# Optimization experiments

Hardware: AMD Instinct MI355X
Metric: run time of the kernel (lower is better)

Reference implementation:

```python
import jax, jax.numpy as jnp
import numpy as np

B, T, I, O = 64, 1024, 512, 512
EPS = 1e-5


def setup_inputs() -> dict:
    key = jax.random.key(0)
    k1, k2 = jax.random.split(key)
    x = jax.random.normal(k1, (B, T, I), dtype=jnp.float32)
    W = jax.random.normal(k2, (4 * O, I + O), dtype=jnp.float32) * 0.02
    gamma = jnp.ones((4, O), dtype=jnp.float32)
    beta = jnp.zeros((4, O), dtype=jnp.float32)
    init_hx = jnp.zeros((1, O), dtype=jnp.float32)
    init_cx = jnp.zeros((1, O), dtype=jnp.float32)
    return {"x": x, "W": W, "gamma": gamma, "beta": beta,
            "init_hx": init_hx, "init_cx": init_cx}


def reference(x, W, gamma, beta, init_hx, init_cx):
    b = x.shape[0]
    o = init_hx.shape[-1]

    def step(carry, xt):
        h, c = carry
        # fused gate projection: [B, I+O] @ [I+O, 4O] -> [B, 4, O]
        z = jnp.concatenate([xt, h], axis=-1) @ W.T
        z = z.reshape(b, 4, o)
        # LayerNorm over the last TWO dims (gate axis + feature axis), per torch nn.LayerNorm([4, O])
        mu = jnp.mean(z, axis=(-2, -1), keepdims=True)
        var = jnp.var(z, axis=(-2, -1), keepdims=True)
        zn = (z - mu) * jax.lax.rsqrt(var + EPS) * gamma + beta
        gates = jax.nn.sigmoid(zn[:, :3])  # f, i, o gates
        f_g, i_g, o_g = gates[:, 0], gates[:, 1], gates[:, 2]
        h_state = jax.nn.gelu(zn[:, 3], approximate=False)  # dropout = identity (eval)
        c_new = f_g * c + i_g * h_state
        h_new = o_g * c_new
        return (h_new, c_new), h_new

    h0 = jnp.broadcast_to(init_hx, (b, o))
    c0 = jnp.broadcast_to(init_cx, (b, o))
    x_t = jnp.swapaxes(x, 0, 1)  # [T, B, I]
    _, hs = jax.lax.scan(step, (h0, c0), x_t)
    return jnp.swapaxes(hs, 0, 1)  # [B, T, O]
```

## Files before the change

### kernel.cpp

```cpp
#include <hip/hip_runtime.h>
#include <math.h>

#define B_  64
#define T_  1024
#define I_  512
#define O_  512
#define NZ  2048
#define KW  1024
#define EPS 1e-5f

#define SREC 32
#define OSL  16

typedef short bf8_t  __attribute__((ext_vector_type(8)));
typedef float f32x4  __attribute__((ext_vector_type(4)));
typedef unsigned uint4v __attribute__((ext_vector_type(4)));

__device__ __forceinline__ unsigned short f2bf(float f) {
  union { float f; unsigned u; } v; v.f = f;
  unsigned r = v.u + 0x7FFFu + ((v.u >> 16) & 1u);
  return (unsigned short)(r >> 16);
}
__device__ __forceinline__ float bf2f(unsigned short b) {
  union { unsigned u; float f; } v; v.u = ((unsigned)b) << 16;
  return v.f;
}

__global__ __launch_bounds__(256) void init_all(
    const float* __restrict__ init_hx,
    unsigned short* __restrict__ h, unsigned* __restrict__ sync) {
  int idx = blockIdx.x * 256 + threadIdx.x;
  if (idx < 2048) sync[idx] = 0u;
  if (idx < B_ * O_) h[idx] = f2bf(init_hx[idx & (O_ - 1)]);
}

__global__ __launch_bounds__(256) void wx_bf16(
    const float* __restrict__ W, unsigned short* __restrict__ Wbf) {
  int idx = blockIdx.x * 256 + threadIdx.x;
  int n  = idx >> 7;
  int k4 = (idx & 127) * 4;
  float4 v = *(const float4*)(W + (size_t)n * KW + k4);
  unsigned short* d = Wbf + (size_t)n * 512 + k4;
  d[0] = f2bf(v.x); d[1] = f2bf(v.y); d[2] = f2bf(v.z); d[3] = f2bf(v.w);
}

__global__ __launch_bounds__(256) void zx_gemm(
    const float* __restrict__ x, const unsigned short* __restrict__ Wbf,
    unsigned short* __restrict__ zx) {
  __shared__ unsigned short xl[64 * 520];
  __shared__ unsigned short cst[64 * 72];

  const int tid  = threadIdx.x;
  const int w    = tid >> 6;
  const int lane = tid & 63;
  const int q    = lane >> 4;
  const int col  = lane & 15;
  const int m0   = blockIdx.x * 64;

  for (int e4 = tid; e4 < 64 * 128; e4 += 256) {
    int r  = e4 >> 7;
    int k4 = (e4 & 127) * 4;
    float4 v = *(const float4*)(x + (size_t)(m0 + r) * I_ + k4);
    unsigned short* d = &xl[r * 520 + k4];
    d[0] = f2bf(v.x); d[1] = f2bf(v.y); d[2] = f2bf(v.z); d[3] = f2bf(v.w);
  }
  __syncthreads();

  const unsigned short* __restrict__ arow = &xl[(16 * w + col) * 520];
  const int crow = tid >> 2;
  const int cc0  = (tid & 3) * 16;

  for (int nblk = 0; nblk < 32; ++nblk) {
    const int n0 = nblk * 64;
    f32x4 acc[4];
    #pragma unroll
    for (int i = 0; i < 4; ++i) acc[i] = (f32x4){0.f, 0.f, 0.f, 0.f};

    #pragma unroll
    for (int ks = 0; ks < 16; ++ks) {
      const int k0 = ks * 32 + q * 8;
      bf8_t af = *(const bf8_t*)(arow + k0);
      #pragma unroll
      for (int nt = 0; nt < 4; ++nt) {
        bf8_t bfr = *(const bf8_t*)(Wbf + (size_t)(n0 + nt * 16 + col) * 512 + k0);
        acc[nt] = __builtin_amdgcn_mfma_f32_16x16x32_bf16(af, bfr, acc[nt], 0, 0, 0);
      }
    }
    __syncthreads();
    #pragma unroll
    for (int nt = 0; nt < 4; ++nt)
      #pragma unroll
      for (int r = 0; r < 4; ++r)
        cst[(16 * w + 4 * q + r) * 72 + nt * 16 + col] = f2bf(acc[nt][r]);
    __syncthreads();
    {
      const uint4v* srcp = (const uint4v*)&cst[crow * 72 + cc0];
      uint4v v0 = srcp[0], v1 = srcp[1];
      uint4v* dst = (uint4v*)&zx[(size_t)(m0 + crow) * NZ + n0 + cc0];
      dst[0] = v0; dst[1] = v1;
    }
  }
}

__global__ __launch_bounds__(256) void lstm_rec(
    const float* __restrict__ W, const float* __restrict__ gamma,
    const float* __restrict__ beta, const float* __restrict__ init_cx,
    const unsigned short* __restrict__ zx, unsigned short* __restrict__ h,
    unsigned long long* __restrict__ part8, float* __restrict__ out,
    unsigned* __restrict__ flags) {

  __shared__ unsigned short whlds[64 * 520];

  const int tid  = threadIdx.x;
  const int w    = tid >> 6;
  const int lane = tid & 63;
  const int q    = lane >> 4;
  const int col  = lane & 15;
  const int s    = blockIdx.x;
  const int o    = s * OSL + col;

  for (int e4 = tid; e4 < 64 * 128; e4 += 256) {
    int r  = e4 >> 7;
    int k4 = (e4 & 127) * 4;
    int g  = r >> 4, np = r & 15;
    const float4 v =
        *(const float4*)(W + (size_t)(512 * g + OSL * s + np) * KW + I_ + k4);
    unsigned short* d = &whlds[r * 520 + k4];
    d[0] = f2bf(v.x); d[1] = f2bf(v.y); d[2] = f2bf(v.z); d[3] = f2bf(v.w);
  }

  float gma[4], bta[4], c_reg[4];
  #pragma unroll
  for (int g = 0; g < 4; ++g) { gma[g] = gamma[g * O_ + o]; bta[g] = beta[g * O_ + o]; }
  { float c0 = init_cx[o];
    #pragma unroll
    for (int r = 0; r < 4; ++r) c_reg[r] = c0; }

  unsigned short zxl[16];
  #pragma unroll
  for (int g = 0; g < 4; ++g)
    #pragma unroll
    for (int r = 0; r < 4; ++r) {
      int b = 16 * w + 4 * q + r;
      zxl[g * 4 + r] = zx[((size_t)b * T_ + 0) * NZ + g * O_ + OSL * s + col];
    }

  __syncthreads();

  for (int t = 0; t < T_; ++t) {
    unsigned long long araw[32];
    const unsigned short* hrow = h + (16 * w + col) * O_;
    #pragma unroll
    for (int ks = 0; ks < 16; ++ks) {
      const unsigned long long* p =
          (const unsigned long long*)(hrow + ks * 32 + q * 8);
      araw[2 * ks]     = __hip_atomic_load(p,     __ATOMIC_RELAXED, __HIP_MEMORY_SCOPE_AGENT);
      araw[2 * ks + 1] = __hip_atomic_load(p + 1, __ATOMIC_RELAXED, __HIP_MEMORY_SCOPE_AGENT);
    }

    f32x4 acc[4];
    #pragma unroll
    for (int g = 0; g < 4; ++g) acc[g] = (f32x4){0.f, 0.f, 0.f, 0.f};

    #pragma unroll
    for (int ks = 0; ks < 16; ++ks) {
      union { unsigned long long u[2]; bf8_t v; } au;
      au.u[0] = araw[2 * ks]; au.u[1] = araw[2 * ks + 1];
      #pragma unroll
      for (int g = 0; g < 4; ++g) {
        bf8_t bfr = *(const bf8_t*)(&whlds[(g * 16 + col) * 520 + ks * 32 + q * 8]);
        acc[g] = __builtin_amdgcn_mfma_f32_16x16x32_bf16(au.v, bfr, acc[g], 0, 0, 0);
      }
    }

    float z[16];
    float s1[4], s2[4];
    #pragma unroll
    for (int r = 0; r < 4; ++r) { s1[r] = 0.f; s2[r] = 0.f; }
    #pragma unroll
    for (int g = 0; g < 4; ++g)
      #pragma unroll
      for (int r = 0; r < 4; ++r) {
        float zv = acc[g][r] + bf2f(zxl[g * 4 + r]);
        z[g * 4 + r] = zv;
        s1[r] += zv;
        s2[r] += zv * zv;
      }
    #pragma unroll
    for (int m = 1; m < 16; m <<= 1) {
      #pragma unroll
      for (int r = 0; r < 4; ++r) {
        s1[r] += __shfl_xor(s1[r], m, 64);
        s2[r] += __shfl_xor(s2[r], m, 64);
      }
    }
    if (col == 0) {
      #pragma unroll
      for (int r = 0; r < 4; ++r) {
        int b = 16 * w + 4 * q + r;
        union { float f[2]; unsigned long long u; } pv;
        pv.f[0] = s1[r]; pv.f[1] = s2[r];
        __hip_atomic_store(&part8[(size_t)s * 64 + b], pv.u,
                           __ATOMIC_RELAXED, __HIP_MEMORY_SCOPE_AGENT);
      }
    }

    __syncthreads();
    {
      const unsigned tgt = 2u * (unsigned)t + 1u;
      if (tid == 0)
        __hip_atomic_store(&flags[s * 16], tgt,
                           __ATOMIC_RELAXED, __HIP_MEMORY_SCOPE_AGENT);
      const unsigned* fp = &flags[(tid & 31) * 16];
      while (__hip_atomic_load(fp, __ATOMIC_RELAXED, __HIP_MEMORY_SCOPE_AGENT) < tgt) {}
    }

    float S1 = 0.f, S2 = 0.f;
    {
      const int brow = 16 * w + (lane & 15);
      const int sbase = (lane >> 4) * 8;
      #pragma unroll
      for (int i = 0; i < 8; ++i) {
        union { float f[2]; unsigned long long u; } pv;
        pv.u = __hip_atomic_load(&part8[(size_t)(sbase + i) * 64 + brow],
                                 __ATOMIC_RELAXED, __HIP_MEMORY_SCOPE_AGENT);
        S1 += pv.f[0]; S2 += pv.f[1];
      }
    }
    S1 += __shfl_xor(S1, 16, 64); S2 += __shfl_xor(S2, 16, 64);
    S1 += __shfl_xor(S1, 32, 64); S2 += __shfl_xor(S2, 32, 64);
    float mean_l = S1 * (1.f / NZ);
    float rstd_l = rsqrtf(S2 * (1.f / NZ) - mean_l * mean_l + EPS);

    float hnl[4];
    #pragma unroll
    for (int r = 0; r < 4; ++r) {
      int b = 16 * w + 4 * q + r;
      float mean = __shfl(mean_l, 4 * q + r, 64);
      float rstd = __shfl(rstd_l, 4 * q + r, 64);
      float zn0 = (z[0 * 4 + r] - mean) * rstd * gma[0] + bta[0];
      float zn1 = (z[1 * 4 + r] - mean) * rstd * gma[1] + bta[1];
      float zn2 = (z[2 * 4 + r] - mean) * rstd * gma[2] + bta[2];
      float zn3 = (z[3 * 4 + r] - mean) * rstd * gma[3] + bta[3];
      float fg = 1.f / (1.f + expf(-zn0));
      float ig = 1.f / (1.f + expf(-zn1));
      float og = 1.f / (1.f + expf(-zn2));
      float gg = 0.5f * zn3 * (1.f + erff(zn3 * 0.70710678118654752f));
      float cn = fg * c_reg[r] + ig * gg;
      float hn = og * cn;
      c_reg[r] = cn;
      hnl[r] = hn;
      __hip_atomic_store(&h[b * O_ + o], f2bf(hn),
                         __ATOMIC_RELAXED, __HIP_MEMORY_SCOPE_AGENT);
    }

    if (t + 1 < T_) {
      __syncthreads();
      const unsigned tgt = 2u * (unsigned)t + 2u;
      if (tid == 0)
        __hip_atomic_store(&flags[s * 16], tgt,
                           __ATOMIC_RELAXED, __HIP_MEMORY_SCOPE_AGENT);
      #pragma unroll
      for (int r = 0; r < 4; ++r) {
        int b = 16 * w + 4 * q + r;
        out[((size_t)b * T_ + t) * O_ + o] = hnl[r];
      }
      #pragma unroll
      for (int g = 0; g < 4; ++g)
        #pragma unroll
        for (int r = 0; r < 4; ++r) {
          int b = 16 * w + 4 * q + r;
          zxl[g * 4 + r] =
              zx[((size_t)b * T_ + (t + 1)) * NZ + g * O_ + OSL * s + col];
        }
      const unsigned* fp = &flags[(tid & 31) * 16];
      while (__hip_atomic_load(fp, __ATOMIC_RELAXED, __HIP_MEMORY_SCOPE_AGENT) < tgt) {}
    } else {
      #pragma unroll
      for (int r = 0; r < 4; ++r) {
        int b = 16 * w + 4 * q + r;
        out[((size_t)b * T_ + t) * O_ + o] = hnl[r];
      }
    }
  }
}

extern "C" void kernel_launch(void* const* d_in, const int* in_sizes, int n_in,
                              void* d_out, int out_size, void* d_ws, size_t ws_size,
                              hipStream_t stream) {
  const float* x       = (const float*)d_in[0];
  const float* W       = (const float*)d_in[1];
  const float* gamma   = (const float*)d_in[2];
  const float* beta    = (const float*)d_in[3];
  const float* init_hx = (const float*)d_in[4];
  const float* init_cx = (const float*)d_in[5];
  float* out = (float*)d_out;
  (void)in_sizes; (void)n_in; (void)out_size; (void)ws_size;

  char* ws = (char*)d_ws;
  unsigned*           flags = (unsigned*)(ws);
  unsigned long long* part8 = (unsigned long long*)(ws + 8192);
  unsigned short*     h     = (unsigned short*)(ws + 32768);
  unsigned short*     Wbf   = (unsigned short*)(ws + (1 << 20));
  unsigned short*     zx    = (unsigned short*)(ws + (4 << 20));

  init_all<<<128, 256, 0, stream>>>(init_hx, h, flags);
  wx_bf16<<<1024, 256, 0, stream>>>(W, Wbf);
  zx_gemm<<<1024, 256, 0, stream>>>(x, Wbf, zx);
  lstm_rec<<<SREC, 256, 0, stream>>>(W, gamma, beta, init_cx, zx, h, part8, out, flags);
}
```

Baseline: 9.497 ms.

## Replace flag barrier for LayerNorm stats with self-validating tagged packets

```diff
diff --git a/kernel.cpp b/kernel.cpp
--- a/kernel.cpp
+++ b/kernel.cpp
@@ -11,6 +11,7 @@
 
 #define SREC 32
 #define OSL  16
+#define BAILOUT (1u << 18)
 
 typedef short bf8_t  __attribute__((ext_vector_type(8)));
 typedef float f32x4  __attribute__((ext_vector_type(4)));
@@ -25,12 +26,17 @@
   union { unsigned u; float f; } v; v.u = ((unsigned)b) << 16;
   return v.f;
 }
+__device__ __forceinline__ float u2f(unsigned u) {
+  union { unsigned u; float f; } v; v.u = u; return v.f;
+}
 
 __global__ __launch_bounds__(256) void init_all(
     const float* __restrict__ init_hx,
-    unsigned short* __restrict__ h, unsigned* __restrict__ sync) {
+    unsigned short* __restrict__ h, unsigned* __restrict__ sync,
+    unsigned* __restrict__ part16) {
   int idx = blockIdx.x * 256 + threadIdx.x;
   if (idx < 2048) sync[idx] = 0u;
+  if (idx < 8192) part16[idx] = 0u;
   if (idx < B_ * O_) h[idx] = f2bf(init_hx[idx & (O_ - 1)]);
 }
 
@@ -106,7 +112,7 @@
     const float* __restrict__ W, const float* __restrict__ gamma,
     const float* __restrict__ beta, const float* __restrict__ init_cx,
     const unsigned short* __restrict__ zx, unsigned short* __restrict__ h,
-    unsigned long long* __restrict__ part8, float* __restrict__ out,
+    unsigned* __restrict__ part16, float* __restrict__ out,
     unsigned* __restrict__ flags) {
 
   __shared__ unsigned short whlds[64 * 520];
@@ -194,38 +200,55 @@
         s2[r] += __shfl_xor(s2[r], m, 64);
       }
     }
+
+    const unsigned tgt = (unsigned)t + 1u;
+
     if (col == 0) {
       #pragma unroll
       for (int r = 0; r < 4; ++r) {
         int b = 16 * w + 4 * q + r;
-        union { float f[2]; unsigned long long u; } pv;
-        pv.f[0] = s1[r]; pv.f[1] = s2[r];
-        __hip_atomic_store(&part8[(size_t)s * 64 + b], pv.u,
-                           __ATOMIC_RELAXED, __HIP_MEMORY_SCOPE_AGENT);
-      }
-    }
-
-    __syncthreads();
-    {
-      const unsigned tgt = 2u * (unsigned)t + 1u;
-      if (tid == 0)
-        __hip_atomic_store(&flags[s * 16], tgt,
-                           __ATOMIC_RELAXED, __HIP_MEMORY_SCOPE_AGENT);
-      const unsigned* fp = &flags[(tid & 31) * 16];
-      while (__hip_atomic_load(fp, __ATOMIC_RELAXED, __HIP_MEMORY_SCOPE_AGENT) < tgt) {}
+        uint4v pkt;
+        pkt[0] = tgt;
+        pkt[1] = __builtin_bit_cast(unsigned, s1[r]);
+        pkt[2] = __builtin_bit_cast(unsigned, s2[r]);
+        pkt[3] = tgt;
+        unsigned* pp = part16 + (size_t)(s * 64 + b) * 4;
+        asm volatile("global_store_dwordx4 %0, %1, off sc1"
+                     :: "v"(pp), "v"(pkt) : "memory");
+      }
     }
 
     float S1 = 0.f, S2 = 0.f;
     {
-      const int brow = 16 * w + (lane & 15);
-      const int sbase = (lane >> 4) * 8;
-      #pragma unroll
-      for (int i = 0; i < 8; ++i) {
-        union { float f[2]; unsigned long long u; } pv;
-        pv.u = __hip_atomic_load(&part8[(size_t)(sbase + i) * 64 + brow],
-                                 __ATOMIC_RELAXED, __HIP_MEMORY_SCOPE_AGENT);
-        S1 += pv.f[0]; S2 += pv.f[1];
-      }
+      const int brow = 16 * w + col;
+      const unsigned* pb  = part16 + ((size_t)q * 512 + brow) * 4;
+      const unsigned* pb2 = pb + 1024;
+      uint4v pk[8];
+      unsigned spins = 0;
+      bool ok;
+      do {
+        asm volatile(
+          "global_load_dwordx4 %0, %8, off sc1\n\t"
+          "global_load_dwordx4 %1, %8, off offset:1024 sc1\n\t"
+          "global_load_dwordx4 %2, %8, off offset:2048 sc1\n\t"
+          "global_load_dwordx4 %3, %8, off offset:3072 sc1\n\t"
+          "global_load_dwordx4 %4, %9, off sc1\n\t"
+          "global_load_dwordx4 %5, %9, off offset:1024 sc1\n\t"
+          "global_load_dwordx4 %6, %9, off offset:2048 sc1\n\t"
+          "global_load_dwordx4 %7, %9, off offset:3072 sc1\n\t"
+          "s_waitcnt vmcnt(0)"
+          : "=&v"(pk[0]), "=&v"(pk[1]), "=&v"(pk[2]), "=&v"(pk[3]),
+            "=&v"(pk[4]), "=&v"(pk[5]), "=&v"(pk[6]), "=&v"(pk[7])
+          : "v"(pb), "v"(pb2)
+          : "memory");
+        ok = true;
+        #pragma unroll
+        for (int i = 0; i < 8; ++i)
+          ok = ok && (pk[i][0] == tgt) && (pk[i][3] == tgt);
+        if (++spins > BAILOUT) break;
+      } while (!__all((int)ok));
+      #pragma unroll
+      for (int i = 0; i < 8; ++i) { S1 += u2f(pk[i][1]); S2 += u2f(pk[i][2]); }
     }
     S1 += __shfl_xor(S1, 16, 64); S2 += __shfl_xor(S2, 16, 64);
     S1 += __shfl_xor(S1, 32, 64); S2 += __shfl_xor(S2, 32, 64);
@@ -256,9 +279,9 @@
 
     if (t + 1 < T_) {
       __syncthreads();
-      const unsigned tgt = 2u * (unsigned)t + 2u;
+      const unsigned ft = 2u * (unsigned)t + 2u;
       if (tid == 0)
-        __hip_atomic_store(&flags[s * 16], tgt,
+        __hip_atomic_store(&flags[s * 16], ft,
                            __ATOMIC_RELAXED, __HIP_MEMORY_SCOPE_AGENT);
       #pragma unroll
       for (int r = 0; r < 4; ++r) {
@@ -274,7 +297,7 @@
               zx[((size_t)b * T_ + (t + 1)) * NZ + g * O_ + OSL * s + col];
         }
       const unsigned* fp = &flags[(tid & 31) * 16];
-      while (__hip_atomic_load(fp, __ATOMIC_RELAXED, __HIP_MEMORY_SCOPE_AGENT) < tgt) {}
+      while (__hip_atomic_load(fp, __ATOMIC_RELAXED, __HIP_MEMORY_SCOPE_AGENT) < ft) {}
     } else {
       #pragma unroll
       for (int r = 0; r < 4; ++r) {
@@ -298,14 +321,14 @@
   (void)in_sizes; (void)n_in; (void)out_size; (void)ws_size;
 
   char* ws = (char*)d_ws;
-  unsigned*           flags = (unsigned*)(ws);
-  unsigned long long* part8 = (unsigned long long*)(ws + 8192);
-  unsigned short*     h     = (unsigned short*)(ws + 32768);
-  unsigned short*     Wbf   = (unsigned short*)(ws + (1 << 20));
-  unsigned short*     zx    = (unsigned short*)(ws + (4 << 20));
-
-  init_all<<<128, 256, 0, stream>>>(init_hx, h, flags);
+  unsigned*       flags  = (unsigned*)(ws);
+  unsigned*       part16 = (unsigned*)(ws + 8192);
+  unsigned short* h      = (unsigned short*)(ws + 49152);
+  unsigned short* Wbf    = (unsigned short*)(ws + (1 << 20));
+  unsigned short* zx     = (unsigned short*)(ws + (4 << 20));
+
+  init_all<<<128, 256, 0, stream>>>(init_hx, h, flags, part16);
   wx_bf16<<<1024, 256, 0, stream>>>(W, Wbf);
   zx_gemm<<<1024, 256, 0, stream>>>(x, Wbf, zx);
-  lstm_rec<<<SREC, 256, 0, stream>>>(W, gamma, beta, init_cx, zx, h, part8, out, flags);
-}
+  lstm_rec<<<SREC, 256, 0, stream>>>(W, gamma, beta, init_cx, zx, h, part16, out, flags);
+}
```

Result: slower. 9.802 ms (+3.2%).

## Fuse input-projection GEMM with recurrence kernel and overlap via per-chunk counters

Applied to the files above, without the earlier changes.

```diff
diff --git a/kernel.cpp b/kernel.cpp
--- a/kernel.cpp
+++ b/kernel.cpp
@@ -10,7 +10,9 @@
 #define EPS 1e-5f
 
 #define SREC 32
+#define NPROD 1024
 #define OSL  16
+#define BAILOUT (1u << 18)
 
 typedef short bf8_t  __attribute__((ext_vector_type(8)));
 typedef float f32x4  __attribute__((ext_vector_type(4)));
@@ -44,80 +46,90 @@
   d[0] = f2bf(v.x); d[1] = f2bf(v.y); d[2] = f2bf(v.z); d[3] = f2bf(v.w);
 }
 
-__global__ __launch_bounds__(256) void zx_gemm(
+__global__ __launch_bounds__(256) void fused_rec(
     const float* __restrict__ x, const unsigned short* __restrict__ Wbf,
-    unsigned short* __restrict__ zx) {
-  __shared__ unsigned short xl[64 * 520];
-  __shared__ unsigned short cst[64 * 72];
+    const float* __restrict__ W, const float* __restrict__ gamma,
+    const float* __restrict__ beta, const float* __restrict__ init_cx,
+    unsigned short* __restrict__ zx, unsigned short* __restrict__ h,
+    unsigned long long* __restrict__ part8, float* __restrict__ out,
+    unsigned* __restrict__ flags) {
+
+  __shared__ unsigned short smem[37888];
 
   const int tid  = threadIdx.x;
   const int w    = tid >> 6;
   const int lane = tid & 63;
   const int q    = lane >> 4;
   const int col  = lane & 15;
-  const int m0   = blockIdx.x * 64;
-
-  for (int e4 = tid; e4 < 64 * 128; e4 += 256) {
-    int r  = e4 >> 7;
-    int k4 = (e4 & 127) * 4;
-    float4 v = *(const float4*)(x + (size_t)(m0 + r) * I_ + k4);
-    unsigned short* d = &xl[r * 520 + k4];
-    d[0] = f2bf(v.x); d[1] = f2bf(v.y); d[2] = f2bf(v.z); d[3] = f2bf(v.w);
+  unsigned* zxcnt = flags + 1024;
+
+  if (blockIdx.x >= SREC) {
+    const int p  = blockIdx.x - SREC;
+    const int b  = p & 63;
+    const int tc = p >> 6;
+    const int m0 = b * T_ + tc * 64;
+
+    unsigned short* xl  = smem;
+    unsigned short* cst = smem + 33280;
+
+    for (int e4 = tid; e4 < 64 * 128; e4 += 256) {
+      int r  = e4 >> 7;
+      int k4 = (e4 & 127) * 4;
+      float4 v = *(const float4*)(x + (size_t)(m0 + r) * I_ + k4);
+      unsigned short* d = &xl[r * 520 + k4];
+      d[0] = f2bf(v.x); d[1] = f2bf(v.y); d[2] = f2bf(v.z); d[3] = f2bf(v.w);
+    }
+    __syncthreads();
+
+    const unsigned short* arow = &xl[(16 * w + col) * 520];
+    const int crow = tid >> 2;
+    const int cc0  = (tid & 3) * 16;
+
+    for (int nblk = 0; nblk < 32; ++nblk) {
+      const int n0 = nblk * 64;
+      f32x4 acc[4];
+      #pragma unroll
+      for (int i = 0; i < 4; ++i) acc[i] = (f32x4){0.f, 0.f, 0.f, 0.f};
+
+      #pragma unroll
+      for (int ks = 0; ks < 16; ++ks) {
+        const int k0 = ks * 32 + q * 8;
+        bf8_t af = *(const bf8_t*)(arow + k0);
+        #pragma unroll
+        for (int nt = 0; nt < 4; ++nt) {
+          bf8_t bfr = *(const bf8_t*)(Wbf + (size_t)(n0 + nt * 16 + col) * 512 + k0);
+          acc[nt] = __builtin_amdgcn_mfma_f32_16x16x32_bf16(af, bfr, acc[nt], 0, 0, 0);
+        }
+      }
+      __syncthreads();
+      #pragma unroll
+      for (int nt = 0; nt < 4; ++nt)
+        #pragma unroll
+        for (int r = 0; r < 4; ++r)
+          cst[(16 * w + 4 * q + r) * 72 + nt * 16 + col] = f2bf(acc[nt][r]);
+      __syncthreads();
+      {
+        union { uint4v v; unsigned long long u[2]; } a0, a1;
+        const uint4v* srcp = (const uint4v*)&cst[crow * 72 + cc0];
+        a0.v = srcp[0]; a1.v = srcp[1];
+        unsigned long long* dst =
+            (unsigned long long*)&zx[(size_t)(m0 + crow) * NZ + n0 + cc0];
+        __hip_atomic_store(dst + 0, a0.u[0], __ATOMIC_RELAXED, __HIP_MEMORY_SCOPE_AGENT);
+        __hip_atomic_store(dst + 1, a0.u[1], __ATOMIC_RELAXED, __HIP_MEMORY_SCOPE_AGENT);
+        __hip_atomic_store(dst + 2, a1.u[0], __ATOMIC_RELAXED, __HIP_MEMORY_SCOPE_AGENT);
+        __hip_atomic_store(dst + 3, a1.u[1], __ATOMIC_RELAXED, __HIP_MEMORY_SCOPE_AGENT);
+      }
+    }
+    __syncthreads();
+    if (tid == 0)
+      __hip_atomic_fetch_add(&zxcnt[tc], 1u, __ATOMIC_RELAXED,
+                             __HIP_MEMORY_SCOPE_AGENT);
+    return;
   }
-  __syncthreads();
-
-  const unsigned short* __restrict__ arow = &xl[(16 * w + col) * 520];
-  const int crow = tid >> 2;
-  const int cc0  = (tid & 3) * 16;
-
-  for (int nblk = 0; nblk < 32; ++nblk) {
-    const int n0 = nblk * 64;
-    f32x4 acc[4];
-    #pragma unroll
-    for (int i = 0; i < 4; ++i) acc[i] = (f32x4){0.f, 0.f, 0.f, 0.f};
-
-    #pragma unroll
-    for (int ks = 0; ks < 16; ++ks) {
-      const int k0 = ks * 32 + q * 8;
-      bf8_t af = *(const bf8_t*)(arow + k0);
-      #pragma unroll
-      for (int nt = 0; nt < 4; ++nt) {
-        bf8_t bfr = *(const bf8_t*)(Wbf + (size_t)(n0 + nt * 16 + col) * 512 + k0);
-        acc[nt] = __builtin_amdgcn_mfma_f32_16x16x32_bf16(af, bfr, acc[nt], 0, 0, 0);
-      }
-    }
-    __syncthreads();
-    #pragma unroll
-    for (int nt = 0; nt < 4; ++nt)
-      #pragma unroll
-      for (int r = 0; r < 4; ++r)
-        cst[(16 * w + 4 * q + r) * 72 + nt * 16 + col] = f2bf(acc[nt][r]);
-    __syncthreads();
-    {
-      const uint4v* srcp = (const uint4v*)&cst[crow * 72 + cc0];
-      uint4v v0 = srcp[0], v1 = srcp[1];
-      uint4v* dst = (uint4v*)&zx[(size_t)(m0 + crow) * NZ + n0 + cc0];
-      dst[0] = v0; dst[1] = v1;
-    }
-  }
-}
-
-__global__ __launch_bounds__(256) void lstm_rec(
-    const float* __restrict__ W, const float* __restrict__ gamma,
-    const float* __restrict__ beta, const float* __restrict__ init_cx,
-    const unsigned short* __restrict__ zx, unsigned short* __restrict__ h,
-    unsigned long long* __restrict__ part8, float* __restrict__ out,
-    unsigned* __restrict__ flags) {
-
-  __shared__ unsigned short whlds[64 * 520];
-
-  const int tid  = threadIdx.x;
-  const int w    = tid >> 6;
-  const int lane = tid & 63;
-  const int q    = lane >> 4;
-  const int col  = lane & 15;
-  const int s    = blockIdx.x;
-  const int o    = s * OSL + col;
+
+  unsigned short* whlds = smem;
+  const int s = blockIdx.x;
+  const int o = s * OSL + col;
 
   for (int e4 = tid; e4 < 64 * 128; e4 += 256) {
     int r  = e4 >> 7;
@@ -136,6 +148,13 @@
     #pragma unroll
     for (int r = 0; r < 4; ++r) c_reg[r] = c0; }
 
+  {
+    unsigned spins = 0;
+    while (__hip_atomic_load(&zxcnt[0], __ATOMIC_RELAXED,
+                             __HIP_MEMORY_SCOPE_AGENT) < 64u) {
+      if (++spins > BAILOUT) break;
+    }
+  }
   unsigned short zxl[16];
   #pragma unroll
   for (int g = 0; g < 4; ++g)
@@ -265,6 +284,14 @@
         int b = 16 * w + 4 * q + r;
         out[((size_t)b * T_ + t) * O_ + o] = hnl[r];
       }
+      if (((t + 1) & 63) == 0) {
+        const int tc = (t + 1) >> 6;
+        unsigned spins = 0;
+        while (__hip_atomic_load(&zxcnt[tc], __ATOMIC_RELAXED,
+                                 __HIP_MEMORY_SCOPE_AGENT) < 64u) {
+          if (++spins > BAILOUT) break;
+        }
+      }
       #pragma unroll
       for (int g = 0; g < 4; ++g)
         #pragma unroll
@@ -306,6 +333,6 @@
 
   init_all<<<128, 256, 0, stream>>>(init_hx, h, flags);
   wx_bf16<<<1024, 256, 0, stream>>>(W, Wbf);
-  zx_gemm<<<1024, 256, 0, stream>>>(x, Wbf, zx);
-  lstm_rec<<<SREC, 256, 0, stream>>>(W, gamma, beta, init_cx, zx, h, part8, out, flags);
-}
+  fused_rec<<<SREC + NPROD, 256, 0, stream>>>(x, Wbf, W, gamma, beta, init_cx,
+                                              zx, h, part8, out, flags);
+}
```

Measured after the change: 9.376 ms. About the same (-1.3%).
